# Kernel optimization log

Measured on AMD Instinct MI355X. Metric: run time of the kernel, lower is better.

Reference implementation:

```python
import jax, jax.numpy as jnp
from jax import lax
import numpy as np

B, C, H, W = 16, 192, 128, 128


def setup_inputs() -> dict:
    key = jax.random.key(0)
    k1, k2, k3 = jax.random.split(key, 3)
    x = jax.random.normal(k1, (B, C, H, W), dtype=jnp.float32)
    # merge = nn.Conv2d(C, C, 1): weight (C, C, 1, 1), bias (C,)
    fan_in = C  # 1x1 kernel
    bound = 1.0 / np.sqrt(fan_in)
    merge_w = jax.random.uniform(k2, (C, C, 1, 1), dtype=jnp.float32, minval=-bound, maxval=bound)
    merge_b = jax.random.uniform(k3, (C,), dtype=jnp.float32, minval=-bound, maxval=bound)
    return {"x": x, "merge_w": merge_w, "merge_b": merge_b}


def reference(x, merge_w, merge_b):
    c = x.shape[1]
    dn = lax.conv_dimension_numbers(x.shape, (c, 1, 3, 3), ('NCHW', 'OIHW', 'NCHW'))
    # Shared 3x3 Laplacian applied per channel == depthwise conv with a
    # broadcast kernel (same math as the per-channel loop in the original).
    lap = jnp.array([[0., -1., 0.], [-1., 4., -1.], [0., -1., 0.]], dtype=x.dtype)
    lap_k = jnp.broadcast_to(lap.reshape(1, 1, 3, 3), (c, 1, 3, 3))
    edges = lax.conv_general_dilated(
        x, lap_k, window_strides=(1, 1), padding=((1, 1), (1, 1)),
        dimension_numbers=dn, feature_group_count=c)
    out = x + edges
    dn1 = lax.conv_dimension_numbers(out.shape, merge_w.shape, ('NCHW', 'OIHW', 'NCHW'))
    y = lax.conv_general_dilated(out, merge_w, window_strides=(1, 1),
                                 padding='VALID', dimension_numbers=dn1)
    return y + merge_b[None, :, None, None]
```

## Files before the change

kernel.cpp:

```cpp
#include <hip/hip_runtime.h>

#define BB   16
#define CC   192
#define HH   128
#define WWD  128
#define HW   16384
#define CHWs (CC * HW)

typedef __attribute__((ext_vector_type(4))) float f4;
typedef __attribute__((ext_vector_type(4))) float f32x4;
typedef __attribute__((ext_vector_type(8))) short bf16x8;

static __device__ __forceinline__ unsigned short f2bf(float f) {
    unsigned u = __float_as_uint(f);
    u += 0x7fffu + ((u >> 16) & 1u);
    return (unsigned short)(u >> 16);
}
static __device__ __forceinline__ float bf2f(unsigned short h) {
    return __uint_as_float(((unsigned)h) << 16);
}

extern "C" __global__ __launch_bounds__(512, 2)
void eeb_kernel(const float* __restrict__ x, const float* __restrict__ wm,
                const float* __restrict__ bias, float* __restrict__ y)
{
    __shared__ __align__(16) char Tl[2][16384];

    const int tid = threadIdx.x;
    const int bid = blockIdx.x;
    const int img = bid >> 6;
    const int r0  = (bid & 63) << 1;

    const int cp = tid >> 5;
    const int sp = tid & 31;
    const int p0 = sp << 3;
    const int w0 = p0 & 127;
    const int rr = r0 + (p0 >> 7);
    const bool upv = (rr > 0), dnv = (rr < 127);
    const int rup = upv ? rr - 1 : rr;
    const int rdn = dnv ? rr + 1 : rr;

    const int lane = tid & 63;
    const int wid  = tid >> 6;
    const int mb = (wid >> 1) * 48;
    const int nb = (wid & 1) * 128;
    const int lr = lane & 15;
    const int lg = lane >> 4;

    const float* xb = x + (size_t)img * CHWs;

    f32x4 acc[3][8];
    #pragma unroll
    for (int i = 0; i < 3; ++i)
        #pragma unroll
        for (int j = 0; j < 8; ++j) acc[i][j] = f32x4{0.f, 0.f, 0.f, 0.f};

    f4 xm[2][2], xu[2][2], xd[2][2];
    float tv[2][8];

    auto LOADX = [&](int kc) {
        #pragma unroll
        for (int ch = 0; ch < 2; ++ch) {
            const float* cb = xb + (size_t)(kc + 2 * cp + ch) * HW;
            const f4* pm = (const f4*)(cb + rr  * WWD + w0);
            const f4* pu = (const f4*)(cb + rup * WWD + w0);
            const f4* pd = (const f4*)(cb + rdn * WWD + w0);
            xm[ch][0] = pm[0]; xm[ch][1] = pm[1];
            xu[ch][0] = pu[0]; xu[ch][1] = pu[1];
            xd[ch][0] = pd[0]; xd[ch][1] = pd[1];
        }
    };
    auto STENCIL = [&]() {
        #pragma unroll
        for (int ch = 0; ch < 2; ++ch) {
            float mm[8], uu[8], dd[8];
            #pragma unroll
            for (int i = 0; i < 8; ++i) {
                mm[i] = xm[ch][i >> 2][i & 3];
                uu[i] = upv ? xu[ch][i >> 2][i & 3] : 0.f;
                dd[i] = dnv ? xd[ch][i >> 2][i & 3] : 0.f;
            }
            float lft = __shfl_up(mm[7], 1);
            float rgt = __shfl_down(mm[0], 1);
            if (w0 == 0)   lft = 0.f;
            if (w0 == 120) rgt = 0.f;
            tv[ch][0] = 5.f * mm[0] - uu[0] - dd[0] - lft - mm[1];
            #pragma unroll
            for (int i = 1; i < 7; ++i)
                tv[ch][i] = 5.f * mm[i] - uu[i] - dd[i] - mm[i - 1] - mm[i + 1];
            tv[ch][7] = 5.f * mm[7] - uu[7] - dd[7] - mm[6] - rgt;
        }
    };

    LOADX(0);
    STENCIL();

    #pragma unroll 1
    for (int kb = 0; kb < 6; ++kb) {
        const int kc = kb * 32;
        __syncthreads();
        #pragma unroll
        for (int i = 0; i < 8; ++i) {
            const int p   = p0 + i;
            const int off = (4 * cp) ^ ((((unsigned)p >> 4) & 3) << 4);
            unsigned short h0 = f2bf(tv[0][i]);
            unsigned short h1 = f2bf(tv[1][i]);
            unsigned short l0 = f2bf(tv[0][i] - bf2f(h0));
            unsigned short l1 = f2bf(tv[1][i] - bf2f(h1));
            *(unsigned*)&Tl[0][p * 64 + off] = (unsigned)h0 | ((unsigned)h1 << 16);
            *(unsigned*)&Tl[1][p * 64 + off] = (unsigned)l0 | ((unsigned)l1 << 16);
        }
        if (kb < 5) LOADX(kc + 32);
        __syncthreads();

        bf16x8 ah[3], al[3];
        #pragma unroll
        for (int mf = 0; mf < 3; ++mf) {
            const float* wp = wm + (size_t)(mb + mf * 16 + lr) * CC + kc + lg * 8;
            f4 wa = *(const f4*)wp;
            f4 wb = *(const f4*)(wp + 4);
            #pragma unroll
            for (int j = 0; j < 8; ++j) {
                float f = (j < 4) ? wa[j] : wb[j - 4];
                unsigned short h = f2bf(f);
                ah[mf][j] = (short)h;
                al[mf][j] = (short)f2bf(f - bf2f(h));
            }
        }
        #pragma unroll
        for (int nf = 0; nf < 8; ++nf) {
            const int pb  = nb + nf * 16;
            const int swz = ((pb >> 4) & 3) << 4;
            const char* rb = &Tl[0][(pb + lr) * 64 + ((16 * lg) ^ swz)];
            bf16x8 bh = *(const bf16x8*)rb;
            bf16x8 bl = *(const bf16x8*)(rb + 16384);
            #pragma unroll
            for (int mf = 0; mf < 3; ++mf) {
                acc[mf][nf] = __builtin_amdgcn_mfma_f32_16x16x32_bf16(ah[mf], bh, acc[mf][nf], 0, 0, 0);
                acc[mf][nf] = __builtin_amdgcn_mfma_f32_16x16x32_bf16(ah[mf], bl, acc[mf][nf], 0, 0, 0);
                acc[mf][nf] = __builtin_amdgcn_mfma_f32_16x16x32_bf16(al[mf], bh, acc[mf][nf], 0, 0, 0);
            }
        }
        if (kb < 5) STENCIL();
    }

    float bv[3][4];
    #pragma unroll
    for (int mf = 0; mf < 3; ++mf)
        #pragma unroll
        for (int r = 0; r < 4; ++r)
            bv[mf][r] = bias[mb + mf * 16 + lg * 4 + r];

    float* yb = y + (size_t)img * CHWs;
    #pragma unroll
    for (int mf = 0; mf < 3; ++mf) {
        #pragma unroll
        for (int nf = 0; nf < 8; ++nf) {
            const int p = nb + nf * 16 + lr;
            float* yp = yb + (size_t)(mb + mf * 16 + lg * 4) * HW
                           + (r0 + (p >> 7)) * WWD + (p & 127);
            #pragma unroll
            for (int r = 0; r < 4; ++r)
                yp[r * HW] = acc[mf][nf][r] + bv[mf][r];
        }
    }
}

extern "C" void kernel_launch(void* const* d_in, const int* in_sizes, int n_in,
                              void* d_out, int out_size, void* d_ws, size_t ws_size,
                              hipStream_t stream)
{
    const float* x  = (const float*)d_in[0];
    const float* wm = (const float*)d_in[1];
    const float* b  = (const float*)d_in[2];
    float* y = (float*)d_out;
    eeb_kernel<<<1024, 512, 0, stream>>>(x, wm, b, y);
}
```

Measured before the change: 406.7 us.

## Pre-split weights into bf16 hi/lo and double-buffer the LDS stencil tile

Adds a small pre-kernel that splits the 1x1 conv weights once into bf16 high and low parts in the workspace, so the main kernel loads ready-made bf16x8 fragments instead of converting fp32 weights in every block and K-step. The LDS tile is double-buffered, which removes one of the two barriers per K-step, and the low-part rounding is replaced by truncation. The launch bound is raised to 4 blocks per CU, but doubling LDS to 64KB per block may stop that occupancy from being reached. Truncating the low part changes the numerics slightly, and there is an extra kernel launch.

```diff
diff --git a/kernel.cpp b/kernel.cpp
--- a/kernel.cpp
+++ b/kernel.cpp
@@ -1,6 +1,5 @@
 #include <hip/hip_runtime.h>
 
-#define BB   16
 #define CC   192
 #define HH   128
 #define WWD  128
@@ -20,11 +19,28 @@
     return __uint_as_float(((unsigned)h) << 16);
 }
 
-extern "C" __global__ __launch_bounds__(512, 2)
-void eeb_kernel(const float* __restrict__ x, const float* __restrict__ wm,
+extern "C" __global__ __launch_bounds__(256)
+void wsplit_kernel(const float* __restrict__ wm,
+                   unsigned short* __restrict__ whi,
+                   unsigned short* __restrict__ wlo)
+{
+    int i = blockIdx.x * 256 + threadIdx.x;
+    if (i < CC * CC) {
+        float f = wm[i];
+        unsigned short h = f2bf(f);
+        float l = f - bf2f(h);
+        whi[i] = h;
+        wlo[i] = (unsigned short)(__float_as_uint(l) >> 16);
+    }
+}
+
+extern "C" __global__ __launch_bounds__(512, 4)
+void eeb_kernel(const float* __restrict__ x,
+                const unsigned short* __restrict__ whi,
+                const unsigned short* __restrict__ wlo,
                 const float* __restrict__ bias, float* __restrict__ y)
 {
-    __shared__ __align__(16) char Tl[2][16384];
+    __shared__ __align__(16) char Tl[2][2][16384];
 
     const int tid = threadIdx.x;
     const int bid = blockIdx.x;
@@ -98,40 +114,33 @@
     #pragma unroll 1
     for (int kb = 0; kb < 6; ++kb) {
         const int kc = kb * 32;
-        __syncthreads();
+        char* Tw = &Tl[kb & 1][0][0];
         #pragma unroll
         for (int i = 0; i < 8; ++i) {
             const int p   = p0 + i;
             const int off = (4 * cp) ^ ((((unsigned)p >> 4) & 3) << 4);
             unsigned short h0 = f2bf(tv[0][i]);
             unsigned short h1 = f2bf(tv[1][i]);
-            unsigned short l0 = f2bf(tv[0][i] - bf2f(h0));
-            unsigned short l1 = f2bf(tv[1][i] - bf2f(h1));
-            *(unsigned*)&Tl[0][p * 64 + off] = (unsigned)h0 | ((unsigned)h1 << 16);
-            *(unsigned*)&Tl[1][p * 64 + off] = (unsigned)l0 | ((unsigned)l1 << 16);
+            unsigned short l0 = (unsigned short)(__float_as_uint(tv[0][i] - bf2f(h0)) >> 16);
+            unsigned short l1 = (unsigned short)(__float_as_uint(tv[1][i] - bf2f(h1)) >> 16);
+            *(unsigned*)&Tw[p * 64 + off]         = (unsigned)h0 | ((unsigned)h1 << 16);
+            *(unsigned*)&Tw[16384 + p * 64 + off] = (unsigned)l0 | ((unsigned)l1 << 16);
         }
+        __syncthreads();
         if (kb < 5) LOADX(kc + 32);
-        __syncthreads();
 
         bf16x8 ah[3], al[3];
         #pragma unroll
         for (int mf = 0; mf < 3; ++mf) {
-            const float* wp = wm + (size_t)(mb + mf * 16 + lr) * CC + kc + lg * 8;
-            f4 wa = *(const f4*)wp;
-            f4 wb = *(const f4*)(wp + 4);
-            #pragma unroll
-            for (int j = 0; j < 8; ++j) {
-                float f = (j < 4) ? wa[j] : wb[j - 4];
-                unsigned short h = f2bf(f);
-                ah[mf][j] = (short)h;
-                al[mf][j] = (short)f2bf(f - bf2f(h));
-            }
+            const size_t wo = (size_t)(mb + mf * 16 + lr) * CC + kc + lg * 8;
+            ah[mf] = *(const bf16x8*)(whi + wo);
+            al[mf] = *(const bf16x8*)(wlo + wo);
         }
         #pragma unroll
         for (int nf = 0; nf < 8; ++nf) {
             const int pb  = nb + nf * 16;
             const int swz = ((pb >> 4) & 3) << 4;
-            const char* rb = &Tl[0][(pb + lr) * 64 + ((16 * lg) ^ swz)];
+            const char* rb = &Tw[(pb + lr) * 64 + ((16 * lg) ^ swz)];
             bf16x8 bh = *(const bf16x8*)rb;
             bf16x8 bl = *(const bf16x8*)(rb + 16384);
             #pragma unroll
@@ -174,5 +183,10 @@
     const float* wm = (const float*)d_in[1];
     const float* b  = (const float*)d_in[2];
     float* y = (float*)d_out;
-    eeb_kernel<<<1024, 512, 0, stream>>>(x, wm, b, y);
+
+    unsigned short* whi = (unsigned short*)d_ws;
+    unsigned short* wlo = whi + CC * CC;
+
+    wsplit_kernel<<<(CC * CC + 255) / 256, 256, 0, stream>>>(wm, whi, wlo);
+    eeb_kernel<<<1024, 512, 0, stream>>>(x, whi, wlo, b, y);
 }
```

Measured after the change: 749.3 us. 1.84x slower.
